# Kernel tuning notes

Hardware: AMD Instinct MI355X
Metric: run time of the kernel (lower is better)

## Reference

```python
import jax, jax.numpy as jnp
import numpy as np

N, D, K = 32768, 256, 2048
BETA = 0.25  # init arg beta, in [0,1) branch of the loss


def setup_inputs() -> dict:
    key = jax.random.key(0)
    k1, k2 = jax.random.split(key)
    x = jax.random.normal(k1, (N, D), dtype=jnp.float32)
    # mimics nn.Embedding init: uniform(-1/K, 1/K) then mean-centered
    cb = jax.random.uniform(k2, (K, D), dtype=jnp.float32, minval=-1.0 / K, maxval=1.0 / K)
    codebook = cb - cb.mean(axis=0)
    return {"x": x, "codebook": codebook}


def reference(x, codebook):
    # pairwise squared L2 distances: [N, K]
    dist = (
        jnp.sum(x * x, axis=1, keepdims=True)
        + jnp.sum(codebook * codebook, axis=1)
        - 2.0 * jnp.matmul(x, codebook.T)
    )
    encoding_inds = jnp.argmin(dist, axis=1)  # [N]
    # one-hot @ codebook == gather of nearest code vectors
    x_codebook = jnp.take(codebook, encoding_inds, axis=0)  # [N, D]
    # straight-through quantization
    x_quantized = x + jax.lax.stop_gradient(x_codebook - x)
    # VQ loss, beta in [0, 1) branch
    commit = jnp.mean((x - jax.lax.stop_gradient(x_codebook)) ** 2)
    embed = jnp.mean((x_codebook - jax.lax.stop_gradient(x)) ** 2)
    loss = BETA * commit + embed
    return x_quantized, loss
```

## Files before the change

### kernel.cpp

```cpp
#include <hip/hip_runtime.h>

#define N_ROWS 32768
#define DIM    256
#define KCODES 2048
#define CSCALE 4096.0f

typedef __attribute__((ext_vector_type(16))) float f32x16;
typedef __attribute__((ext_vector_type(4)))  unsigned int u32x4;

union frag16 { u32x4 v; long l[2]; };

#define WAIT_LGKM0 0xC07F
#define WAIT_VM4   0x0F74
#define WAIT_VM0   0x0F70

__device__ __forceinline__ void gl16(const void* g, void* l) {
    __builtin_amdgcn_global_load_lds(
        (const __attribute__((address_space(1))) unsigned int*)g,
        (__attribute__((address_space(3))) unsigned int*)l, 16, 0, 0);
}

__device__ __forceinline__ uint4 pack16(const float* s) {
    int a = __builtin_amdgcn_cvt_pk_fp8_f32(s[0],  s[1],  0, false);
    a     = __builtin_amdgcn_cvt_pk_fp8_f32(s[2],  s[3],  a, true);
    int b = __builtin_amdgcn_cvt_pk_fp8_f32(s[4],  s[5],  0, false);
    b     = __builtin_amdgcn_cvt_pk_fp8_f32(s[6],  s[7],  b, true);
    int c = __builtin_amdgcn_cvt_pk_fp8_f32(s[8],  s[9],  0, false);
    c     = __builtin_amdgcn_cvt_pk_fp8_f32(s[10], s[11], c, true);
    int d = __builtin_amdgcn_cvt_pk_fp8_f32(s[12], s[13], 0, false);
    d     = __builtin_amdgcn_cvt_pk_fp8_f32(s[14], s[15], d, true);
    uint4 o; o.x = a; o.y = b; o.z = c; o.w = d;
    return o;
}


__global__ void prep_cb(const float* __restrict__ cb, unsigned int* __restrict__ cbf8,
                        float* __restrict__ halfcn, float* __restrict__ loss) {
    const int t    = threadIdx.x;
    const int code = blockIdx.x * 4 + (t >> 6);
    const int s    = t & 63;
    if (blockIdx.x == 0 && t == 0) *loss = 0.0f;
    const int kc = s >> 4, d = (s >> 2) & 3, b4 = (s & 3) * 4;
    const int h = d >> 1, q = d & 1;
    const int k0 = kc * 64 + q * 32 + (b4 >> 3) * 16 + h * 8 + (b4 & 7);
    float4 v = *(const float4*)&cb[(size_t)code * DIM + k0];
    int pk = __builtin_amdgcn_cvt_pk_fp8_f32(v.x * CSCALE, v.y * CSCALE, 0, false);
    pk     = __builtin_amdgcn_cvt_pk_fp8_f32(v.z * CSCALE, v.w * CSCALE, pk, true);
    cbf8[(size_t)code * 64 + s] = (unsigned int)pk;
    float ssum = v.x * v.x + v.y * v.y + v.z * v.z + v.w * v.w;
    #pragma unroll
    for (int o = 32; o > 0; o >>= 1) ssum += __shfl_down(ssum, o, 64);
    if (s == 0) halfcn[code] = 0.5f * CSCALE * ssum;
}

__global__ __launch_bounds__(256, 2) void vq_fused(
        const float* __restrict__ x, const float* __restrict__ cb,
        const char* __restrict__ cbf8, const float* __restrict__ halfcn,
        float* __restrict__ out, float* __restrict__ loss) {
    __shared__ char As[4][4096];
    __shared__ char Bs[2][4][4096];
    __shared__ float red[64][4];
    __shared__ int  idxs[64];
    __shared__ float lred[4];

    const int t    = threadIdx.x;
    const int lane = t & 63;
    const int w    = t >> 6;
    const int l32  = lane & 31;
    const int h    = lane >> 5;
    const int row0 = blockIdx.x * 64;

    {
        const int r   = t >> 2;
        const int kc  = t & 3;
        const int key = (r >> 1) & 3;
        const float* src = x + (size_t)(row0 + r) * DIM + kc * 64;
        float buf[16];
        #pragma unroll
        for (int p = 0; p < 4; p++) {
            const int d = p ^ key, hh = d >> 1, qq = d & 1;
            #pragma unroll
            for (int j = 0; j < 4; j++) *(float4*)(buf + j * 4) =
                *(const float4*)(src + qq * 32 + (j >> 1) * 16 + hh * 8 + (j & 1) * 4);
            *(uint4*)(As[kc] + r * 64 + p * 16) = pack16(buf);
        }
    }

    float hcv[8][2];
    #pragma unroll
    for (int p = 0; p < 8; p++) {
        hcv[p][0] = halfcn[p * 256 + w * 64 + l32];
        hcv[p][1] = halfcn[p * 256 + w * 64 + 32 + l32];
    }

    const int lsub = lane >> 2;
    const int lpos = lane & 3;
    auto stageB = [&](int i) {
        const int pass = i >> 2, kc = i & 3;
        char* dst = Bs[i & 1][w];
        #pragma unroll
        for (int r_ = 0; r_ < 4; r_++) {
            const int lc = r_ * 16 + lsub;
            const int g  = lpos ^ ((lc >> 1) & 3);
            const char* src = cbf8 + (size_t)(pass * 256 + w * 64 + lc) * 256
                              + kc * 64 + g * 16;
            gl16(src, dst + r_ * 1024);
        }
    };

    const int key = (l32 >> 1) & 3;
    const int p0  = (h * 2 + 0) ^ key;
    const int p1  = (h * 2 + 1) ^ key;

    frag16 af[2][2][2], bf[2][2][2];

    float mp[2][16];
    #pragma unroll
    for (int rt = 0; rt < 2; rt++)
        #pragma unroll
        for (int r = 0; r < 16; r++) mp[rt][r] = -3.0e38f;

    __syncthreads();

    stageB(0);
    stageB(1);
    __builtin_amdgcn_s_waitcnt(WAIT_VM4);
    {
        const char* ab = As[0];
        const char* bb = Bs[0][w];
        #pragma unroll
        for (int rt = 0; rt < 2; rt++) {
            const int rbase = (rt * 32 + l32) * 64;
            af[0][rt][0].v = *(const u32x4*)(ab + rbase + p0 * 16);
            af[0][rt][1].v = *(const u32x4*)(ab + rbase + p1 * 16);
        }
        #pragma unroll
        for (int ct = 0; ct < 2; ct++) {
            const int cbase = (ct * 32 + l32) * 64;
            bf[0][ct][0].v = *(const u32x4*)(bb + cbase + p0 * 16);
            bf[0][ct][1].v = *(const u32x4*)(bb + cbase + p1 * 16);
        }
    }

    for (int pass = 0; pass < 8; ++pass) {
        f32x16 acc[2][2];
        #pragma unroll
        for (int rt = 0; rt < 2; rt++)
            #pragma unroll
            for (int r = 0; r < 16; r++) {
                acc[rt][0][r] = -hcv[pass][0];
                acc[rt][1][r] = -hcv[pass][1];
            }

        #pragma unroll
        for (int kc = 0; kc < 4; ++kc) {
            const int i   = pass * 4 + kc;
            const int cs  = kc & 1;
            const int ns  = cs ^ 1;

            __builtin_amdgcn_s_waitcnt(WAIT_LGKM0);

            if (i + 2 < 32) {
                stageB(i + 2);
                __builtin_amdgcn_s_waitcnt(WAIT_VM4);
            } else if (i + 1 < 32) {
                __builtin_amdgcn_s_waitcnt(WAIT_VM0);
            }

            if (i + 1 < 32) {
                const char* ab = As[(kc + 1) & 3];
                const char* bb = Bs[(i + 1) & 1][w];
                #pragma unroll
                for (int rt = 0; rt < 2; rt++) {
                    const int rbase = (rt * 32 + l32) * 64;
                    af[ns][rt][0].v = *(const u32x4*)(ab + rbase + p0 * 16);
                    af[ns][rt][1].v = *(const u32x4*)(ab + rbase + p1 * 16);
                }
                #pragma unroll
                for (int ct = 0; ct < 2; ct++) {
                    const int cbase = (ct * 32 + l32) * 64;
                    bf[ns][ct][0].v = *(const u32x4*)(bb + cbase + p0 * 16);
                    bf[ns][ct][1].v = *(const u32x4*)(bb + cbase + p1 * 16);
                }
            }

            #pragma unroll
            for (int q = 0; q < 2; q++)
                #pragma unroll
                for (int hf = 0; hf < 2; hf++)
                    #pragma unroll
                    for (int rt = 0; rt < 2; rt++)
                        #pragma unroll
                        for (int ct = 0; ct < 2; ct++)
                            acc[rt][ct] = __builtin_amdgcn_mfma_f32_32x32x16_fp8_fp8(
                                af[cs][rt][q].l[hf], bf[cs][ct][q].l[hf],
                                acc[rt][ct], 0, 0, 0);
        }

        #pragma unroll
        for (int ct = 0; ct < 2; ct++) {
            const unsigned code = (unsigned)(pass * 256 + w * 64 + ct * 32 + l32);
            #pragma unroll
            for (int rt = 0; rt < 2; rt++)
                #pragma unroll
                for (int r = 0; r < 16; r++) {
                    unsigned u = (__float_as_uint(acc[rt][ct][r]) & 0xFFFFF800u) | code;
                    mp[rt][r] = fmaxf(mp[rt][r], __uint_as_float(u));
                }
        }
    }

    #pragma unroll
    for (int m = 1; m <= 16; m <<= 1)
        #pragma unroll
        for (int rt = 0; rt < 2; rt++)
            #pragma unroll
            for (int r = 0; r < 16; r++)
                mp[rt][r] = fmaxf(mp[rt][r], __shfl_xor(mp[rt][r], m, 64));

    if (l32 == 0) {
        #pragma unroll
        for (int rt = 0; rt < 2; rt++)
            #pragma unroll
            for (int r = 0; r < 16; r++) {
                const int row = rt * 32 + (r & 3) + 8 * (r >> 2) + 4 * h;
                red[row][w] = mp[rt][r];
            }
    }
    __syncthreads();
    if (t < 64) {
        float b0 = fmaxf(fmaxf(red[t][0], red[t][1]), fmaxf(red[t][2], red[t][3]));
        idxs[t] = (int)(__float_as_uint(b0) & 2047u);
    }
    __syncthreads();

    float lsum = 0.0f;
    #pragma unroll 4
    for (int r = 0; r < 64; r++) {
        const int code = idxs[r];
        const float c  = cb[(size_t)code * DIM + t];
        const float xv = x[(size_t)(row0 + r) * DIM + t];
        out[(size_t)(row0 + r) * DIM + t] = c;
        const float d = xv - c;
        lsum += d * d;
    }
    #pragma unroll
    for (int o = 32; o > 0; o >>= 1) lsum += __shfl_down(lsum, o, 64);
    if (lane == 0) lred[w] = lsum;
    __syncthreads();
    if (t == 0) {
        const float scale = 1.25f / (float)((size_t)N_ROWS * DIM);
        atomicAdd(loss, (lred[0] + lred[1] + lred[2] + lred[3]) * scale);
    }
}

extern "C" void kernel_launch(void* const* d_in, const int* in_sizes, int n_in,
                              void* d_out, int out_size, void* d_ws, size_t ws_size,
                              hipStream_t stream) {
    const float* x  = (const float*)d_in[0];
    const float* cb = (const float*)d_in[1];
    float* out  = (float*)d_out;
    float* loss = out + (size_t)N_ROWS * DIM;

    char* ws = (char*)d_ws;
    unsigned int* cbf8 = (unsigned int*)ws;
    float* halfcn = (float*)(ws + (size_t)KCODES * 256);

    prep_cb<<<KCODES / 4, 256, 0, stream>>>(cb, cbf8, halfcn, loss);
    vq_fused<<<N_ROWS / 64, 256, 0, stream>>>(x, cb, (const char*)cbf8, halfcn, out, loss);
}
```

Measured before the change: 123.4 us.

## Hold A fragments in registers and triple-buffer codebook tiles in LDS

The x-tile fragments for all four K-chunks are loaded once into registers instead of being re-read from LDS every step. Codebook staging moves from double to triple buffering, so prefetch runs two chunks ahead. The half-norms are staged through shared memory instead of 16 per-thread registers, and the loop now uses inline-asm ds_read_b128, sched_barrier and setprio around the MFMA bursts. The goal is fewer LDS reads and better hiding of global-load latency, at the cost of more registers and LDS, which could reduce occupancy, and of fragile hand-written waitcnt logic.

```diff
diff --git a/kernel.cpp b/kernel.cpp
--- a/kernel.cpp
+++ b/kernel.cpp
@@ -10,14 +10,20 @@
 
 union frag16 { u32x4 v; long l[2]; };
 
-#define WAIT_LGKM0 0xC07F
-#define WAIT_VM4   0x0F74
-#define WAIT_VM0   0x0F70
+#define SWAIT(s) asm volatile("s_waitcnt " s)
 
 __device__ __forceinline__ void gl16(const void* g, void* l) {
     __builtin_amdgcn_global_load_lds(
         (const __attribute__((address_space(1))) unsigned int*)g,
         (__attribute__((address_space(3))) unsigned int*)l, 16, 0, 0);
+}
+
+__device__ __forceinline__ u32x4 ldsr128(const void* p) {
+    const unsigned a =
+        (unsigned)(unsigned long long)(__attribute__((address_space(3))) const char*)p;
+    u32x4 d;
+    asm volatile("ds_read_b128 %0, %1" : "=&v"(d) : "v"(a));
+    return d;
 }
 
 __device__ __forceinline__ uint4 pack16(const float* s) {
@@ -58,7 +64,8 @@
         const char* __restrict__ cbf8, const float* __restrict__ halfcn,
         float* __restrict__ out, float* __restrict__ loss) {
     __shared__ char As[4][4096];
-    __shared__ char Bs[2][4][4096];
+    __shared__ char Bs[3][4][4096];
+    __shared__ float hcs[KCODES];
     __shared__ float red[64][4];
     __shared__ int  idxs[64];
     __shared__ float lred[4];
@@ -84,26 +91,21 @@
                 *(const float4*)(src + qq * 32 + (j >> 1) * 16 + hh * 8 + (j & 1) * 4);
             *(uint4*)(As[kc] + r * 64 + p * 16) = pack16(buf);
         }
-    }
-
-    float hcv[8][2];
-    #pragma unroll
-    for (int p = 0; p < 8; p++) {
-        hcv[p][0] = halfcn[p * 256 + w * 64 + l32];
-        hcv[p][1] = halfcn[p * 256 + w * 64 + 32 + l32];
+        #pragma unroll
+        for (int j = 0; j < 8; j++) hcs[j * 256 + t] = halfcn[j * 256 + t];
     }
 
     const int lsub = lane >> 2;
     const int lpos = lane & 3;
-    auto stageB = [&](int i) {
-        const int pass = i >> 2, kc = i & 3;
-        char* dst = Bs[i & 1][w];
+    auto stageB = [&](int j) {
+        const int pass_ = j >> 2, kc_ = j & 3;
+        char* dst = Bs[j % 3][w];
         #pragma unroll
         for (int r_ = 0; r_ < 4; r_++) {
             const int lc = r_ * 16 + lsub;
             const int g  = lpos ^ ((lc >> 1) & 3);
-            const char* src = cbf8 + (size_t)(pass * 256 + w * 64 + lc) * 256
-                              + kc * 64 + g * 16;
+            const char* src = cbf8 + (size_t)(pass_ * 256 + w * 64 + lc) * 256
+                              + kc_ * 64 + g * 16;
             gl16(src, dst + r_ * 1024);
         }
     };
@@ -112,7 +114,8 @@
     const int p0  = (h * 2 + 0) ^ key;
     const int p1  = (h * 2 + 1) ^ key;
 
-    frag16 af[2][2][2], bf[2][2][2];
+    frag16 afr[4][2][2];
+    frag16 bf[2][2][2];
 
     float mp[2][16];
     #pragma unroll
@@ -122,68 +125,71 @@
 
     __syncthreads();
 
-    stageB(0);
-    stageB(1);
-    __builtin_amdgcn_s_waitcnt(WAIT_VM4);
-    {
-        const char* ab = As[0];
-        const char* bb = Bs[0][w];
+    #pragma unroll
+    for (int kc = 0; kc < 4; kc++) {
+        const char* ab = As[kc];
         #pragma unroll
         for (int rt = 0; rt < 2; rt++) {
             const int rbase = (rt * 32 + l32) * 64;
-            af[0][rt][0].v = *(const u32x4*)(ab + rbase + p0 * 16);
-            af[0][rt][1].v = *(const u32x4*)(ab + rbase + p1 * 16);
-        }
+            afr[kc][rt][0].v = *(const u32x4*)(ab + rbase + p0 * 16);
+            afr[kc][rt][1].v = *(const u32x4*)(ab + rbase + p1 * 16);
+        }
+    }
+
+    stageB(0); stageB(1); stageB(2);
+    SWAIT("vmcnt(8)");
+    {
+        const char* bb = Bs[0][w];
         #pragma unroll
         for (int ct = 0; ct < 2; ct++) {
             const int cbase = (ct * 32 + l32) * 64;
-            bf[0][ct][0].v = *(const u32x4*)(bb + cbase + p0 * 16);
-            bf[0][ct][1].v = *(const u32x4*)(bb + cbase + p1 * 16);
-        }
-    }
-
+            bf[0][ct][0].v = ldsr128(bb + cbase + p0 * 16);
+            bf[0][ct][1].v = ldsr128(bb + cbase + p1 * 16);
+        }
+    }
+
+    #pragma unroll
     for (int pass = 0; pass < 8; ++pass) {
+        const float hc0 = hcs[pass * 256 + w * 64 + l32];
+        const float hc1 = hcs[pass * 256 + w * 64 + 32 + l32];
         f32x16 acc[2][2];
         #pragma unroll
         for (int rt = 0; rt < 2; rt++)
             #pragma unroll
             for (int r = 0; r < 16; r++) {
-                acc[rt][0][r] = -hcv[pass][0];
-                acc[rt][1][r] = -hcv[pass][1];
+                acc[rt][0][r] = -hc0;
+                acc[rt][1][r] = -hc1;
             }
 
         #pragma unroll
         for (int kc = 0; kc < 4; ++kc) {
-            const int i   = pass * 4 + kc;
-            const int cs  = kc & 1;
-            const int ns  = cs ^ 1;
-
-            __builtin_amdgcn_s_waitcnt(WAIT_LGKM0);
-
-            if (i + 2 < 32) {
-                stageB(i + 2);
-                __builtin_amdgcn_s_waitcnt(WAIT_VM4);
-            } else if (i + 1 < 32) {
-                __builtin_amdgcn_s_waitcnt(WAIT_VM0);
+            const int i  = pass * 4 + kc;
+            const int cs = kc & 1;
+            const int ns = cs ^ 1;
+
+            SWAIT("lgkmcnt(0)");
+            __builtin_amdgcn_sched_barrier(0);
+
+            if (i + 3 < 32) {
+                stageB(i + 3);
+                SWAIT("vmcnt(8)");
+            } else if (i == 29) {
+                SWAIT("vmcnt(4)");
+            } else if (i == 30) {
+                SWAIT("vmcnt(0)");
             }
 
             if (i + 1 < 32) {
-                const char* ab = As[(kc + 1) & 3];
-                const char* bb = Bs[(i + 1) & 1][w];
-                #pragma unroll
-                for (int rt = 0; rt < 2; rt++) {
-                    const int rbase = (rt * 32 + l32) * 64;
-                    af[ns][rt][0].v = *(const u32x4*)(ab + rbase + p0 * 16);
-                    af[ns][rt][1].v = *(const u32x4*)(ab + rbase + p1 * 16);
-                }
+                const char* bb = Bs[(i + 1) % 3][w];
                 #pragma unroll
                 for (int ct = 0; ct < 2; ct++) {
                     const int cbase = (ct * 32 + l32) * 64;
-                    bf[ns][ct][0].v = *(const u32x4*)(bb + cbase + p0 * 16);
-                    bf[ns][ct][1].v = *(const u32x4*)(bb + cbase + p1 * 16);
+                    bf[ns][ct][0].v = ldsr128(bb + cbase + p0 * 16);
+                    bf[ns][ct][1].v = ldsr128(bb + cbase + p1 * 16);
                 }
             }
 
+            __builtin_amdgcn_s_setprio(1);
             #pragma unroll
             for (int q = 0; q < 2; q++)
                 #pragma unroll
@@ -193,8 +199,9 @@
                         #pragma unroll
                         for (int ct = 0; ct < 2; ct++)
                             acc[rt][ct] = __builtin_amdgcn_mfma_f32_32x32x16_fp8_fp8(
-                                af[cs][rt][q].l[hf], bf[cs][ct][q].l[hf],
+                                afr[kc][rt][q].l[hf], bf[cs][ct][q].l[hf],
                                 acc[rt][ct], 0, 0, 0);
+            __builtin_amdgcn_s_setprio(0);
         }
 
         #pragma unroll
```

After: 125.2 us. No clear change (+1.5%).
